# Kernel optimization log

Measured on AMD Instinct MI355X. Metric: run time of the kernel, lower is better.

## Reference

```python
import jax, jax.numpy as jnp
import numpy as np

T, B, F, H, C = 128, 64, 512, 1024, 513


def _tess_big(W):
    # W: (4, d_in/4, d_out/4) components (r, i, j, k).
    # Tessarine product (commutative): i^2=-1, j^2=+1, k=ij, k^2=-1.
    # Equivalent real block matrix so x @ bigW computes the tessarine linear.
    Wr, Wi, Wj, Wk = W[0], W[1], W[2], W[3]
    return jnp.concatenate([
        jnp.concatenate([Wr,  Wi,  Wj,  Wk], axis=1),
        jnp.concatenate([-Wi, Wr, -Wk,  Wj], axis=1),
        jnp.concatenate([Wj,  Wk,  Wr,  Wi], axis=1),
        jnp.concatenate([-Wk, Wj, -Wi,  Wr], axis=1),
    ], axis=0)  # (d_in, d_out)


def setup_inputs() -> dict:
    key = jax.random.key(0)
    ks = jax.random.split(key, 16)

    def w(k, din, dout):
        return (jax.random.normal(k, (4, din // 4, dout // 4), jnp.float32)
                / np.float32(np.sqrt(din)))

    return {
        "x": jax.random.normal(ks[0], (T, B, F), jnp.float32),
        "wfx_W": w(ks[1], F, H), "wfx_b": jnp.zeros((H,), jnp.float32),
        "wfh_W": w(ks[2], H, H),
        "wix_W": w(ks[3], F, H), "wix_b": jnp.zeros((H,), jnp.float32),
        "wih_W": w(ks[4], H, H),
        "wox_W": w(ks[5], F, H), "wox_b": jnp.zeros((H,), jnp.float32),
        "woh_W": w(ks[6], H, H),
        "wcx_W": w(ks[7], F, H), "wcx_b": jnp.zeros((H,), jnp.float32),
        "wch_W": w(ks[8], H, H),
        "fco_W": jax.random.normal(ks[9], (H, C), jnp.float32) / np.float32(np.sqrt(H)),
        "fco_b": jnp.zeros((C,), jnp.float32),
    }


def reference(x, wfx_W, wfx_b, wfh_W, wix_W, wix_b, wih_W,
              wox_W, wox_b, woh_W, wcx_W, wcx_b, wch_W, fco_W, fco_b):
    Tn, Bn, _ = x.shape
    Hd = wfh_W.shape[1] * 4

    # Precompute input-to-hidden tessarine linears for all timesteps: (T, B, H)
    gx_f = x @ _tess_big(wfx_W) + wfx_b
    gx_i = x @ _tess_big(wix_W) + wix_b
    gx_o = x @ _tess_big(wox_W) + wox_b
    gx_c = x @ _tess_big(wcx_W) + wcx_b

    Wfh = _tess_big(wfh_W)
    Wih = _tess_big(wih_W)
    Woh = _tess_big(woh_W)
    Wch = _tess_big(wch_W)

    def step(carry, g):
        h, c = carry
        fx, ix, ox, cx = g
        ft = jax.nn.sigmoid(fx + h @ Wfh)
        it = jax.nn.sigmoid(ix + h @ Wih)
        ot = jax.nn.sigmoid(ox + h @ Woh)
        at = cx + h @ Wch
        c = it * jnp.tanh(at) + ft * c
        h = ot * jnp.tanh(c)
        return (h, c), None

    h0 = jnp.zeros((Bn, Hd), x.dtype)
    (h, _), _ = jax.lax.scan(step, (h0, h0), (gx_f, gx_i, gx_o, gx_c))
    return h @ fco_W + fco_b  # (B, num_classes)
```

## Files before the change

kernel.cpp:

```cpp
#include <hip/hip_runtime.h>
#include <hip/hip_cooperative_groups.h>

typedef short bfv8 __attribute__((ext_vector_type(8)));
typedef float fv4  __attribute__((ext_vector_type(4)));
typedef unsigned long long u64;

#define T_STEPS 128
#define BATCH   64
#define FDIM    512
#define HDIM    1024
#define NCOL    4096
#define NCLS    513
#define HSLOT   65536

#define PREP_N0 4194304
#define PREP_N1 2097152
#define PREP_N2 4194304
#define PREP_N3 4096
#define PREP_TOTAL (PREP_N0 + PREP_N1 + PREP_N2 + PREP_N3)

static __device__ __forceinline__ float b2f(unsigned short u) {
  union { unsigned int i; float f; } v; v.i = ((unsigned int)u) << 16; return v.f;
}
static __device__ __forceinline__ unsigned short f2b(float f) {
  union { float f; unsigned int i; } v; v.f = f;
  unsigned int r = v.i + 0x7FFFu + ((v.i >> 16) & 1u);
  return (unsigned short)(r >> 16);
}
static __device__ __forceinline__ float sigm(float x) { return 1.0f / (1.0f + __expf(-x)); }
static __device__ __forceinline__ float tanh_f(float x) {
  float e = __expf(-2.0f * fabsf(x));
  float t = (1.0f - e) / (1.0f + e);
  return x >= 0.0f ? t : -t;
}

__global__ void detect_k(const unsigned short* __restrict__ xr, int* __restrict__ flag) {
  __shared__ int cnt;
  if (threadIdx.x == 0) cnt = 0;
  __syncthreads();
  int local = 0;
  for (int s = 0; s < 4; ++s) {
    int i = threadIdx.x + 256 * s;
    unsigned short u = xr[2 * i];
    int e = (u >> 7) & 0xFF;
    if (e >= 112 && e <= 131) local++;
  }
  atomicAdd(&cnt, local);
  __syncthreads();
  if (threadIdx.x == 0) *flag = (cnt >= 512) ? 1 : 0;
}

__global__ void prep_k(const void* __restrict__ x,
                       const void* w0x, const void* w1x, const void* w2x, const void* w3x,
                       const void* w0h, const void* w1h, const void* w2h, const void* w3h,
                       const void* b0, const void* b1, const void* b2, const void* b3,
                       const int* __restrict__ flagp,
                       unsigned short* __restrict__ xbf,
                       unsigned short* __restrict__ WXT,
                       unsigned short* __restrict__ WHT,
                       float* __restrict__ biasI) {
  int fl = *flagp;
  long idx = (long)blockIdx.x * 256 + threadIdx.x;
  if (idx < PREP_N0) {
    int i = (int)idx;
    xbf[i] = fl ? ((const unsigned short*)x)[i] : f2b(((const float*)x)[i]);
    return;
  }
  idx -= PREP_N0;
  if (idx < PREP_N1) {
    int i = (int)idx;
    int n = i >> 9, k = i & 511;
    int j = n >> 2, g = n & 3;
    int rb = k >> 7, p = k & 127;
    int cb = j >> 8, q = j & 255;
    int comp = rb ^ cb;
    int neg = (rb & 1) && !(cb & 1);
    const void* W = (g == 0) ? w0x : (g == 1) ? w1x : (g == 2) ? w2x : w3x;
    int off = comp * (128 * 256) + p * 256 + q;
    unsigned short v;
    if (fl) { v = ((const unsigned short*)W)[off]; if (neg) v ^= 0x8000u; }
    else    { float f = ((const float*)W)[off]; if (neg) f = -f; v = f2b(f); }
    WXT[i] = v;
    return;
  }
  idx -= PREP_N1;
  if (idx < PREP_N2) {
    int i = (int)idx;
    int n = i >> 10, k = i & 1023;
    int j = n >> 2, g = n & 3;
    int rb = k >> 8, p = k & 255;
    int cb = j >> 8, q = j & 255;
    int comp = rb ^ cb;
    int neg = (rb & 1) && !(cb & 1);
    const void* W = (g == 0) ? w0h : (g == 1) ? w1h : (g == 2) ? w2h : w3h;
    int off = comp * (256 * 256) + p * 256 + q;
    unsigned short v;
    if (fl) { v = ((const unsigned short*)W)[off]; if (neg) v ^= 0x8000u; }
    else    { float f = ((const float*)W)[off]; if (neg) f = -f; v = f2b(f); }
    WHT[i] = v;
    return;
  }
  idx -= PREP_N2;
  {
    int i = (int)idx;
    int j = i >> 2, g = i & 3;
    const void* B = (g == 0) ? b0 : (g == 1) ? b1 : (g == 2) ? b2 : b3;
    biasI[i] = fl ? b2f(((const unsigned short*)B)[j]) : ((const float*)B)[j];
  }
}

__global__ void __launch_bounds__(256, 1) phaseB_k(const unsigned short* __restrict__ xbf,
                                                   const unsigned short* __restrict__ WXT,
                                                   const unsigned short* __restrict__ WHT,
                                                   const float* __restrict__ biasI,
                                                   unsigned short* __restrict__ hring,
                                                   int* __restrict__ flags) {
  __shared__ unsigned short Wh[64][1032];
  __shared__ float Pl[4][16][16];
  __shared__ __align__(16) unsigned short Hp[16][16];
  int tid = threadIdx.x;
  int grp = blockIdx.x >> 6;
  int blk = blockIdx.x & 63;
  int n0  = blk * 64;
  for (int c = tid; c < 64 * 128; c += 256) {
    int row = c >> 7, ch = c & 127;
    *(uint4*)&Wh[row][ch * 8] = *(const uint4*)&WHT[(size_t)(n0 + row) * HDIM + ch * 8];
  }
  __syncthreads();
  int w = tid >> 6, lane = tid & 63;
  int col = lane & 15, quad = lane >> 4;
  int gbatch = grp * 16 + col;
  const unsigned short* whp = &Wh[w * 16 + col][quad * 8];
  const unsigned short* wxp = WXT + (size_t)(n0 + w * 16 + col) * FDIM + quad * 8;
  float4 bv = *(const float4*)&biasI[n0 + w * 16 + quad * 4];
  int* myflag   = flags + (grp * 64 + blk) * 16;
  int* pollflag = flags + (grp * 64 + lane) * 16;
  size_t fbase = (size_t)grp * 16384 + (size_t)(quad >> 1) * 256
               + (size_t)col * 16 + (size_t)(quad & 1) * 8;
  size_t pregion = (size_t)grp * 16384 + (size_t)blk * 256;
  float creg = 0.0f;
  fv4 gx0 = {0.f, 0.f, 0.f, 0.f}, gx1 = {0.f, 0.f, 0.f, 0.f};
  {
    const unsigned short* xrow = xbf + (size_t)gbatch * FDIM + quad * 8;
#pragma unroll
    for (int k0 = 0; k0 < FDIM; k0 += 64) {
      bfv8 a0 = *(const bfv8*)(xrow + k0);
      bfv8 b0 = *(const bfv8*)(wxp + k0);
      bfv8 a1 = *(const bfv8*)(xrow + k0 + 32);
      bfv8 b1 = *(const bfv8*)(wxp + k0 + 32);
      gx0 = __builtin_amdgcn_mfma_f32_16x16x32_bf16(a0, b0, gx0, 0, 0, 0);
      gx1 = __builtin_amdgcn_mfma_f32_16x16x32_bf16(a1, b1, gx1, 0, 0, 0);
    }
  }
  for (int t = 0; t < T_STEPS; ++t) {
    const unsigned short* hin  = hring + (size_t)t * HSLOT;
    unsigned short*       hout = hring + (size_t)(t + 1) * HSLOT;
    const uint4* hq = (const uint4*)(hin + fbase);
    uint4 hs[32];
#pragma unroll
    for (int f = 0; f < 32; ++f) hs[f] = hq[f * 64];
    if (w == 0 && t > 0) {
      fv4 g0 = {0.f, 0.f, 0.f, 0.f}, g1 = {0.f, 0.f, 0.f, 0.f};
      const unsigned short* xrow = xbf + (size_t)(t * BATCH + gbatch) * FDIM + quad * 8;
#pragma unroll
      for (int k0 = 0; k0 < FDIM; k0 += 64) {
        bfv8 a0v = *(const bfv8*)(xrow + k0);
        bfv8 b0v = *(const bfv8*)(wxp + k0);
        bfv8 a1v = *(const bfv8*)(xrow + k0 + 32);
        bfv8 b1v = *(const bfv8*)(wxp + k0 + 32);
        g0 = __builtin_amdgcn_mfma_f32_16x16x32_bf16(a0v, b0v, g0, 0, 0, 0);
        g1 = __builtin_amdgcn_mfma_f32_16x16x32_bf16(a1v, b1v, g1, 0, 0, 0);
      }
      gx0 = g0; gx1 = g1;
    }
    fv4 acc0 = gx0, acc1 = gx1;
    fv4 acc2 = {0.f, 0.f, 0.f, 0.f}, acc3 = {0.f, 0.f, 0.f, 0.f};
#pragma unroll
    for (int f = 0; f < 32; f += 4) {
      union { uint4 q; bfv8 v; } u0, u1, u2, u3;
      u0.q = hs[f];     u1.q = hs[f + 1];
      u2.q = hs[f + 2]; u3.q = hs[f + 3];
      bfv8 b0 = *(const bfv8*)(whp + f * 32);
      bfv8 b1 = *(const bfv8*)(whp + (f + 1) * 32);
      bfv8 b2 = *(const bfv8*)(whp + (f + 2) * 32);
      bfv8 b3 = *(const bfv8*)(whp + (f + 3) * 32);
      acc0 = __builtin_amdgcn_mfma_f32_16x16x32_bf16(u0.v, b0, acc0, 0, 0, 0);
      acc1 = __builtin_amdgcn_mfma_f32_16x16x32_bf16(u1.v, b1, acc1, 0, 0, 0);
      acc2 = __builtin_amdgcn_mfma_f32_16x16x32_bf16(u2.v, b2, acc2, 0, 0, 0);
      acc3 = __builtin_amdgcn_mfma_f32_16x16x32_bf16(u3.v, b3, acc3, 0, 0, 0);
    }
    fv4 acc = (acc0 + acc1) + (acc2 + acc3);
#pragma unroll
    for (int r = 0; r < 4; ++r) Pl[w][quad * 4 + r][col] = acc[r];
    asm volatile("" ::: "memory");
    __builtin_amdgcn_s_waitcnt(0);
    asm volatile("" ::: "memory");
    float4 pv = *(const float4*)&Pl[w][col][quad * 4];
    float fg = sigm(pv.x + bv.x);
    float ig = sigm(pv.y + bv.y);
    float og = sigm(pv.z + bv.z);
    float av = pv.w + bv.w;
    float cn = ig * tanh_f(av) + fg * creg;
    float hn = og * tanh_f(cn);
    creg = cn;
    Hp[col][w * 4 + quad] = f2b(hn);
    __syncthreads();
    if (w == 0) {
      u64 pk = ((const u64*)&Hp[0][0])[lane];
      __hip_atomic_store((u64*)(hout + pregion) + lane, pk,
                         __ATOMIC_RELAXED, __HIP_MEMORY_SCOPE_AGENT);
    }
    if (t + 1 < T_STEPS) {
      if (w == 0) {
        asm volatile("s_waitcnt vmcnt(0)" ::: "memory");
        if (lane == 0)
          __hip_atomic_store(myflag, t + 1, __ATOMIC_RELAXED, __HIP_MEMORY_SCOPE_AGENT);
        u64 done = 0;
        for (;;) {
          int v = 0;
          if (!((done >> lane) & 1))
            v = __hip_atomic_load(pollflag, __ATOMIC_RELAXED, __HIP_MEMORY_SCOPE_AGENT);
          done |= __ballot(v >= t + 1);
          if (done == ~0ull) break;
          __builtin_amdgcn_s_sleep(1);
        }
      } else {
        fv4 g0 = {0.f, 0.f, 0.f, 0.f}, g1 = {0.f, 0.f, 0.f, 0.f};
        const unsigned short* xrow = xbf + (size_t)((t + 1) * BATCH + gbatch) * FDIM + quad * 8;
#pragma unroll
        for (int k0 = 0; k0 < FDIM; k0 += 64) {
          bfv8 a0v = *(const bfv8*)(xrow + k0);
          bfv8 b0v = *(const bfv8*)(wxp + k0);
          bfv8 a1v = *(const bfv8*)(xrow + k0 + 32);
          bfv8 b1v = *(const bfv8*)(wxp + k0 + 32);
          g0 = __builtin_amdgcn_mfma_f32_16x16x32_bf16(a0v, b0v, g0, 0, 0, 0);
          g1 = __builtin_amdgcn_mfma_f32_16x16x32_bf16(a1v, b1v, g1, 0, 0, 0);
        }
        gx0 = g0; gx1 = g1;
      }
      __syncthreads();
    }
  }
}

__global__ void phaseC_k(const unsigned short* __restrict__ h,
                         const void* __restrict__ fw, const void* __restrict__ fb,
                         const int* __restrict__ flagp, void* __restrict__ out) {
  int idx = blockIdx.x * 256 + threadIdx.x;
  if (idx >= BATCH * NCLS) return;
  int b = idx / NCLS, cc = idx - b * NCLS;
  const unsigned short* hr = h + (size_t)(b >> 4) * 16384 + (size_t)(b & 15) * 16;
  float acc = 0.f;
  if (*flagp) {
    const unsigned short* fwp = (const unsigned short*)fw;
    for (int k = 0; k < HDIM; ++k)
      acc = fmaf(b2f(hr[((k >> 4) << 8) + (k & 15)]), b2f(fwp[k * NCLS + cc]), acc);
    acc += b2f(((const unsigned short*)fb)[cc]);
    ((unsigned short*)out)[idx] = f2b(acc);
  } else {
    const float* fwp = (const float*)fw;
    for (int k = 0; k < HDIM; ++k)
      acc = fmaf(b2f(hr[((k >> 4) << 8) + (k & 15)]), fwp[k * NCLS + cc], acc);
    acc += ((const float*)fb)[cc];
    ((float*)out)[idx] = acc;
  }
}

extern "C" void kernel_launch(void* const* d_in, const int* in_sizes, int n_in,
                              void* d_out, int out_size, void* d_ws, size_t ws_size,
                              hipStream_t stream) {
  const void* x   = d_in[0];
  const void* wfx = d_in[1];  const void* bfv = d_in[2];  const void* wfh = d_in[3];
  const void* wix = d_in[4];  const void* biv = d_in[5];  const void* wih = d_in[6];
  const void* wox = d_in[7];  const void* bov = d_in[8];  const void* woh = d_in[9];
  const void* wcx = d_in[10]; const void* bcv = d_in[11]; const void* wch = d_in[12];
  const void* fcw = d_in[13]; const void* fcb = d_in[14];

  char* ws = (char*)d_ws;
  int*            flag  = (int*)           (ws);
  unsigned short* WXT   = (unsigned short*)(ws + 256);
  unsigned short* WHT   = (unsigned short*)(ws + 4194560);
  float*          biasI = (float*)         (ws + 12583168);
  unsigned short* xbf   = (unsigned short*)(ws + 12599552);
  unsigned short* hring = (unsigned short*)(ws + 20988160);
  int*            flags = (int*)           (ws + 37896448);

  detect_k<<<1, 256, 0, stream>>>((const unsigned short*)x, flag);
  prep_k<<<PREP_TOTAL / 256, 256, 0, stream>>>(x, wfx, wix, wox, wcx,
                                               wfh, wih, woh, wch,
                                               bfv, biv, bov, bcv,
                                               flag, xbf, WXT, WHT, biasI);
  hipMemsetAsync(hring, 0, 131072, stream);
  hipMemsetAsync(flags, 0, 16384, stream);

  const unsigned short* p_x = xbf;
  const unsigned short* p_wx = WXT;
  const unsigned short* p_wh = WHT;
  const float* p_bi = biasI;
  unsigned short* p_hr = hring;
  int* p_fl = flags;
  void* kargs[] = { (void*)&p_x, (void*)&p_wx, (void*)&p_wh, (void*)&p_bi,
                    (void*)&p_hr, (void*)&p_fl };
  hipLaunchCooperativeKernel((void*)phaseB_k, dim3(256), dim3(256), kargs, 0, stream);

  phaseC_k<<<(BATCH * NCLS + 255) / 256, 256, 0, stream>>>(hring + 128 * HSLOT, fcw, fcb,
                                                           flag, d_out);
}
```

Baseline: 988.7 us.

## Fuse output projection into recurrent kernel, fold memsets into prep, restructure step wait

The separate phaseC output-projection kernel is removed. Each block of the cooperative recurrent kernel now computes a slice of the final h @ fco_W + fco_b after the last step, with a two-half reduction through shared memory. The hring and flags zeroing moves from hipMemsetAsync into extra ranges of prep_k. All four warps now compute the next step's input projection and then each warp polls the group flags itself, replacing the split where warp 0 polled while the other warps did the input GEMM. The aim is to cut launch count and tail latency, at the cost of more flag polling traffic and fewer block-wide barriers inside the loop.

```diff
diff --git a/kernel.cpp b/kernel.cpp
--- a/kernel.cpp
+++ b/kernel.cpp
@@ -9,7 +9,6 @@
 #define BATCH   64
 #define FDIM    512
 #define HDIM    1024
-#define NCOL    4096
 #define NCLS    513
 #define HSLOT   65536
 
@@ -17,7 +16,9 @@
 #define PREP_N1 2097152
 #define PREP_N2 4194304
 #define PREP_N3 4096
-#define PREP_TOTAL (PREP_N0 + PREP_N1 + PREP_N2 + PREP_N3)
+#define PREP_N4 65536
+#define PREP_N5 4096
+#define PREP_TOTAL (PREP_N0 + PREP_N1 + PREP_N2 + PREP_N3 + PREP_N4 + PREP_N5)
 
 static __device__ __forceinline__ float b2f(unsigned short u) {
   union { unsigned int i; float f; } v; v.i = ((unsigned int)u) << 16; return v.f;
@@ -58,7 +59,9 @@
                        unsigned short* __restrict__ xbf,
                        unsigned short* __restrict__ WXT,
                        unsigned short* __restrict__ WHT,
-                       float* __restrict__ biasI) {
+                       float* __restrict__ biasI,
+                       unsigned short* __restrict__ hring0,
+                       int* __restrict__ flags) {
   int fl = *flagp;
   long idx = (long)blockIdx.x * 256 + threadIdx.x;
   if (idx < PREP_N0) {
@@ -101,12 +104,38 @@
     return;
   }
   idx -= PREP_N2;
-  {
+  if (idx < PREP_N3) {
     int i = (int)idx;
     int j = i >> 2, g = i & 3;
     const void* B = (g == 0) ? b0 : (g == 1) ? b1 : (g == 2) ? b2 : b3;
     biasI[i] = fl ? b2f(((const unsigned short*)B)[j]) : ((const float*)B)[j];
-  }
+    return;
+  }
+  idx -= PREP_N3;
+  if (idx < PREP_N4) { hring0[(int)idx] = 0; return; }
+  idx -= PREP_N4;
+  flags[(int)idx] = 0;
+}
+
+static __device__ __forceinline__ float dot512_tail(const unsigned short* __restrict__ hfin,
+                                                    const void* __restrict__ fw, int fl,
+                                                    int b, int col, int half) {
+  float s = 0.f;
+  int k0 = half * 512;
+  if (fl) {
+    const unsigned short* fwp = (const unsigned short*)fw;
+#pragma unroll 8
+    for (int k = k0; k < k0 + 512; ++k)
+      s = fmaf(b2f(hfin[((k >> 4) << 8) + b * 16 + (k & 15)]),
+               b2f(fwp[k * NCLS + col]), s);
+  } else {
+    const float* fwp = (const float*)fw;
+#pragma unroll 8
+    for (int k = k0; k < k0 + 512; ++k)
+      s = fmaf(b2f(hfin[((k >> 4) << 8) + b * 16 + (k & 15)]),
+               fwp[k * NCLS + col], s);
+  }
+  return s;
 }
 
 __global__ void __launch_bounds__(256, 1) phaseB_k(const unsigned short* __restrict__ xbf,
@@ -114,11 +143,17 @@
                                                    const unsigned short* __restrict__ WHT,
                                                    const float* __restrict__ biasI,
                                                    unsigned short* __restrict__ hring,
-                                                   int* __restrict__ flags) {
+                                                   int* __restrict__ flags,
+                                                   const int* __restrict__ flagp,
+                                                   const void* __restrict__ fcw,
+                                                   const void* __restrict__ fcb,
+                                                   void* __restrict__ out) {
   __shared__ unsigned short Wh[64][1032];
   __shared__ float Pl[4][16][16];
   __shared__ __align__(16) unsigned short Hp[16][16];
+  __shared__ float Cred[128];
   int tid = threadIdx.x;
+  int fl = *flagp;
   int grp = blockIdx.x >> 6;
   int blk = blockIdx.x & 63;
   int n0  = blk * 64;
@@ -159,20 +194,6 @@
     uint4 hs[32];
 #pragma unroll
     for (int f = 0; f < 32; ++f) hs[f] = hq[f * 64];
-    if (w == 0 && t > 0) {
-      fv4 g0 = {0.f, 0.f, 0.f, 0.f}, g1 = {0.f, 0.f, 0.f, 0.f};
-      const unsigned short* xrow = xbf + (size_t)(t * BATCH + gbatch) * FDIM + quad * 8;
-#pragma unroll
-      for (int k0 = 0; k0 < FDIM; k0 += 64) {
-        bfv8 a0v = *(const bfv8*)(xrow + k0);
-        bfv8 b0v = *(const bfv8*)(wxp + k0);
-        bfv8 a1v = *(const bfv8*)(xrow + k0 + 32);
-        bfv8 b1v = *(const bfv8*)(wxp + k0 + 32);
-        g0 = __builtin_amdgcn_mfma_f32_16x16x32_bf16(a0v, b0v, g0, 0, 0, 0);
-        g1 = __builtin_amdgcn_mfma_f32_16x16x32_bf16(a1v, b1v, g1, 0, 0, 0);
-      }
-      gx0 = g0; gx1 = g1;
-    }
     fv4 acc0 = gx0, acc1 = gx1;
     fv4 acc2 = {0.f, 0.f, 0.f, 0.f}, acc3 = {0.f, 0.f, 0.f, 0.f};
 #pragma unroll
@@ -209,60 +230,69 @@
       u64 pk = ((const u64*)&Hp[0][0])[lane];
       __hip_atomic_store((u64*)(hout + pregion) + lane, pk,
                          __ATOMIC_RELAXED, __HIP_MEMORY_SCOPE_AGENT);
-    }
+      asm volatile("s_waitcnt vmcnt(0)" ::: "memory");
+      if (lane == 0)
+        __hip_atomic_store(myflag, t + 1, __ATOMIC_RELAXED, __HIP_MEMORY_SCOPE_AGENT);
+    }
+    asm volatile("" ::: "memory");
     if (t + 1 < T_STEPS) {
-      if (w == 0) {
-        asm volatile("s_waitcnt vmcnt(0)" ::: "memory");
-        if (lane == 0)
-          __hip_atomic_store(myflag, t + 1, __ATOMIC_RELAXED, __HIP_MEMORY_SCOPE_AGENT);
-        u64 done = 0;
-        for (;;) {
-          int v = 0;
-          if (!((done >> lane) & 1))
-            v = __hip_atomic_load(pollflag, __ATOMIC_RELAXED, __HIP_MEMORY_SCOPE_AGENT);
-          done |= __ballot(v >= t + 1);
-          if (done == ~0ull) break;
-          __builtin_amdgcn_s_sleep(1);
-        }
-      } else {
-        fv4 g0 = {0.f, 0.f, 0.f, 0.f}, g1 = {0.f, 0.f, 0.f, 0.f};
-        const unsigned short* xrow = xbf + (size_t)((t + 1) * BATCH + gbatch) * FDIM + quad * 8;
-#pragma unroll
-        for (int k0 = 0; k0 < FDIM; k0 += 64) {
-          bfv8 a0v = *(const bfv8*)(xrow + k0);
-          bfv8 b0v = *(const bfv8*)(wxp + k0);
-          bfv8 a1v = *(const bfv8*)(xrow + k0 + 32);
-          bfv8 b1v = *(const bfv8*)(wxp + k0 + 32);
-          g0 = __builtin_amdgcn_mfma_f32_16x16x32_bf16(a0v, b0v, g0, 0, 0, 0);
-          g1 = __builtin_amdgcn_mfma_f32_16x16x32_bf16(a1v, b1v, g1, 0, 0, 0);
-        }
-        gx0 = g0; gx1 = g1;
+      fv4 g0 = {0.f, 0.f, 0.f, 0.f}, g1 = {0.f, 0.f, 0.f, 0.f};
+      const unsigned short* xrow = xbf + (size_t)((t + 1) * BATCH + gbatch) * FDIM + quad * 8;
+#pragma unroll
+      for (int k0 = 0; k0 < FDIM; k0 += 64) {
+        bfv8 a0v = *(const bfv8*)(xrow + k0);
+        bfv8 b0v = *(const bfv8*)(wxp + k0);
+        bfv8 a1v = *(const bfv8*)(xrow + k0 + 32);
+        bfv8 b1v = *(const bfv8*)(wxp + k0 + 32);
+        g0 = __builtin_amdgcn_mfma_f32_16x16x32_bf16(a0v, b0v, g0, 0, 0, 0);
+        g1 = __builtin_amdgcn_mfma_f32_16x16x32_bf16(a1v, b1v, g1, 0, 0, 0);
       }
+      gx0 = g0; gx1 = g1;
+    }
+    asm volatile("" ::: "memory");
+    u64 done = 0;
+    for (;;) {
+      int v = 0;
+      if (!((done >> lane) & 1))
+        v = __hip_atomic_load(pollflag, __ATOMIC_RELAXED, __HIP_MEMORY_SCOPE_AGENT);
+      done |= __ballot(v >= t + 1);
+      if (done == ~0ull) break;
+      __builtin_amdgcn_s_sleep(1);
+    }
+    asm volatile("" ::: "memory");
+  }
+  {
+    const unsigned short* hfin = hring + (size_t)T_STEPS * HSLOT + (size_t)grp * 16384;
+    int b    = tid & 15;
+    int cc   = (tid >> 4) & 7;
+    int half = tid >> 7;
+    int colm = blk * 8 + cc;
+    float s = dot512_tail(hfin, fcw, fl, b, colm, half);
+    if (half) Cred[tid & 127] = s;
+    __syncthreads();
+    if (!half) {
+      float r = s + Cred[tid];
+      float bias = fl ? b2f(((const unsigned short*)fcb)[colm])
+                      : ((const float*)fcb)[colm];
+      r += bias;
+      int oidx = (grp * 16 + b) * NCLS + colm;
+      if (fl) ((unsigned short*)out)[oidx] = f2b(r);
+      else    ((float*)out)[oidx] = r;
+    }
+    if (blk == 63) {
+      float s2 = 0.f;
+      if (tid < 32) s2 = dot512_tail(hfin, fcw, fl, tid & 15, 512, tid >> 4);
       __syncthreads();
-    }
-  }
-}
-
-__global__ void phaseC_k(const unsigned short* __restrict__ h,
-                         const void* __restrict__ fw, const void* __restrict__ fb,
-                         const int* __restrict__ flagp, void* __restrict__ out) {
-  int idx = blockIdx.x * 256 + threadIdx.x;
-  if (idx >= BATCH * NCLS) return;
-  int b = idx / NCLS, cc = idx - b * NCLS;
-  const unsigned short* hr = h + (size_t)(b >> 4) * 16384 + (size_t)(b & 15) * 16;
-  float acc = 0.f;
-  if (*flagp) {
-    const unsigned short* fwp = (const unsigned short*)fw;
-    for (int k = 0; k < HDIM; ++k)
-      acc = fmaf(b2f(hr[((k >> 4) << 8) + (k & 15)]), b2f(fwp[k * NCLS + cc]), acc);
-    acc += b2f(((const unsigned short*)fb)[cc]);
-    ((unsigned short*)out)[idx] = f2b(acc);
-  } else {
-    const float* fwp = (const float*)fw;
-    for (int k = 0; k < HDIM; ++k)
-      acc = fmaf(b2f(hr[((k >> 4) << 8) + (k & 15)]), fwp[k * NCLS + cc], acc);
-    acc += ((const float*)fb)[cc];
-    ((float*)out)[idx] = acc;
+      if (tid < 32 && (tid >> 4)) Cred[tid & 15] = s2;
+      __syncthreads();
+      if (tid < 16) {
+        float r = s2 + Cred[tid];
+        r += fl ? b2f(((const unsigned short*)fcb)[512]) : ((const float*)fcb)[512];
+        int oidx = (grp * 16 + tid) * NCLS + 512;
+        if (fl) ((unsigned short*)out)[oidx] = f2b(r);
+        else    ((float*)out)[oidx] = r;
+      }
+    }
   }
 }
 
@@ -289,9 +319,8 @@
   prep_k<<<PREP_TOTAL / 256, 256, 0, stream>>>(x, wfx, wix, wox, wcx,
                                                wfh, wih, woh, wch,
                                                bfv, biv, bov, bcv,
-                                               flag, xbf, WXT, WHT, biasI);
-  hipMemsetAsync(hring, 0, 131072, stream);
-  hipMemsetAsync(flags, 0, 16384, stream);
+                                               flag, xbf, WXT, WHT, biasI,
+                                               hring, flags);
 
   const unsigned short* p_x = xbf;
   const unsigned short* p_wx = WXT;
@@ -299,10 +328,12 @@
   const float* p_bi = biasI;
   unsigned short* p_hr = hring;
   int* p_fl = flags;
+  const int* p_flag = flag;
+  const void* p_fcw = fcw;
+  const void* p_fcb = fcb;
+  void* p_out = d_out;
   void* kargs[] = { (void*)&p_x, (void*)&p_wx, (void*)&p_wh, (void*)&p_bi,
-                    (void*)&p_hr, (void*)&p_fl };
+                    (void*)&p_hr, (void*)&p_fl, (void*)&p_flag,
+                    (void*)&p_fcw, (void*)&p_fcb, (void*)&p_out };
   hipLaunchCooperativeKernel((void*)phaseB_k, dim3(256), dim3(256), kargs, 0, stream);
-
-  phaseC_k<<<(BATCH * NCLS + 255) / 256, 256, 0, stream>>>(hring + 128 * HSLOT, fcw, fcb,
-                                                           flag, d_out);
-}
+}
```

Measured after the change: 1.048 ms. +6.0%, slower.
